# Performance work log

Measured on AMD Instinct MI355X. Metric: run time of the kernel, lower is better.

## Reference

```python
import jax, jax.numpy as jnp
from jax import lax
import numpy as np

B, T, H, W = 8, 32, 128, 128
D_MODEL, D_STATE, D_CONV, EXPAND = 256, 16, 4, 2
D_INNER = EXPAND * D_MODEL
DT_RANK = 16  # ceil(d_model/16)
CHANS = [3, 32, 64, 96]
COV_SCALE = 0.01


def setup_inputs() -> dict:
    key = jax.random.key(0)
    ks = iter(jax.random.split(key, 64))
    def n(shape, s=0.02):
        return jax.random.normal(next(ks), shape, dtype=jnp.float32) * s
    inp = {
        "frames": jax.random.normal(next(ks), (B, T, 3, H, W), dtype=jnp.float32),
        "target_bboxes": jax.random.uniform(next(ks), (B, T, 4), dtype=jnp.float32),
    }
    for i in range(3):
        inp[f"conv_w{i}"] = n((CHANS[i + 1], CHANS[i], 3, 3, 3))
        inp[f"conv_b{i}"] = jnp.zeros((CHANS[i + 1],), jnp.float32)
        inp[f"bn_g{i}"] = jnp.ones((CHANS[i + 1],), jnp.float32)
        inp[f"bn_b{i}"] = jnp.zeros((CHANS[i + 1],), jnp.float32)
    inp["ep_w"] = n((D_MODEL, CHANS[-1])); inp["ep_b"] = jnp.zeros((D_MODEL,), jnp.float32)
    inp["bp1_w"] = n((64, 4), 0.1); inp["bp1_b"] = jnp.zeros((64,), jnp.float32)
    inp["bp2_w"] = n((D_MODEL, 64)); inp["bp2_b"] = jnp.zeros((D_MODEL,), jnp.float32)
    inp["in_proj_w"] = n((2 * D_INNER, D_MODEL))
    inp["conv1d_w"] = n((D_INNER, 1, D_CONV), 0.1)
    inp["conv1d_b"] = jnp.zeros((D_INNER,), jnp.float32)
    inp["x_proj_w"] = n((DT_RANK + 2 * D_STATE, D_INNER))
    inp["dt_proj_w"] = n((D_INNER, DT_RANK), 0.1)
    inp["dt_proj_b"] = jnp.full((D_INNER,), -3.0, jnp.float32)
    inp["A_log"] = jnp.log(jnp.broadcast_to(jnp.arange(1, D_STATE + 1, dtype=jnp.float32), (D_INNER, D_STATE)))
    inp["D_param"] = jnp.ones((D_INNER,), jnp.float32)
    inp["out_proj_w"] = n((D_MODEL, D_INNER))
    inp["h1_w"] = n((D_MODEL // 2, D_MODEL)); inp["h1_b"] = jnp.zeros((D_MODEL // 2,), jnp.float32)
    inp["h2_w"] = n((4, D_MODEL // 2), 0.1); inp["h2_b"] = jnp.zeros((4,), jnp.float32)
    inp["kf_F"] = jnp.eye(4, dtype=jnp.float32) + n((4, 4), 0.01)
    inp["kf_H"] = jnp.eye(4, dtype=jnp.float32) + n((4, 4), 0.01)
    inp["kf_log_q"] = n((4,), 1.0) - 2.0
    inp["kf_log_r"] = n((4,), 1.0) - 2.0
    return inp


DN3D = ("NCDHW", "OIDHW", "NCDHW")


def _forward(frames, target_bboxes, conv_w0, conv_b0, bn_g0, bn_b0,
             conv_w1, conv_b1, bn_g1, bn_b1, conv_w2, conv_b2, bn_g2, bn_b2,
             ep_w, ep_b, bp1_w, bp1_b, bp2_w, bp2_b,
             in_proj_w, conv1d_w, conv1d_b, x_proj_w, dt_proj_w, dt_proj_b,
             A_log, D_param, out_proj_w, h1_w, h1_b, h2_w, h2_b,
             kf_F, kf_H, kf_log_q, kf_log_r):
    Bn, Tn = frames.shape[0], frames.shape[1]

    # ---- bbox_proj: Linear(4,64) -> ReLU -> Linear(64,d_model) ----
    bf = jax.nn.relu(target_bboxes @ bp1_w.T + bp1_b) @ bp2_w.T + bp2_b  # (B,T,Dm)

    # ---- 3D conv encoder (BN in eval mode: running stats 0/1 -> affine only) ----
    x = jnp.transpose(frames, (0, 2, 1, 3, 4))  # (B,C,T,H,W)
    for (w, b, g, be) in ((conv_w0, conv_b0, bn_g0, bn_b0),
                          (conv_w1, conv_b1, bn_g1, bn_b1),
                          (conv_w2, conv_b2, bn_g2, bn_b2)):
        x = lax.conv_general_dilated(x, w, (1, 2, 2), ((1, 1), (1, 1), (1, 1)),
                                     dimension_numbers=DN3D) + b[None, :, None, None, None]
        x = g[None, :, None, None, None] * x + be[None, :, None, None, None]
        x = jax.nn.relu(x)
        x = lax.reduce_window(x, -jnp.inf, lax.max, (1, 1, 1, 2, 2), (1, 1, 1, 2, 2), "VALID")
    x = x.mean(axis=(3, 4))                    # AdaptiveAvgPool3d((None,1,1)) -> (B,Cenc,T)
    ff = jnp.transpose(x, (0, 2, 1)) @ ep_w.T + ep_b  # (B,T,Dm)

    u = ff + bf

    # ---- Mamba block ----
    xz = u @ in_proj_w.T                        # (B,T,2*Di)
    xm, z = jnp.split(xz, 2, axis=-1)
    xc = jnp.transpose(xm, (0, 2, 1))           # (B,Di,T)
    xc = lax.conv_general_dilated(xc, conv1d_w, (1,), ((D_CONV - 1, 0),),
                                  dimension_numbers=("NCW", "OIW", "NCW"),
                                  feature_group_count=D_INNER) + conv1d_b[None, :, None]
    xs = jax.nn.silu(jnp.transpose(xc, (0, 2, 1)))  # (B,T,Di)
    xdbl = xs @ x_proj_w.T
    dt, Bm, Cm = jnp.split(xdbl, [DT_RANK, DT_RANK + D_STATE], axis=-1)
    dt = jax.nn.softplus(dt @ dt_proj_w.T + dt_proj_b)    # (B,T,Di)
    A = -jnp.exp(A_log)                                    # (Di,Ds)
    dA = jnp.exp(dt[..., None] * A)                        # (B,T,Di,Ds)
    dBx = dt[..., None] * Bm[:, :, None, :] * xs[..., None]

    def ssm_step(h, inputs):
        dA_t, dBx_t, C_t = inputs
        h = dA_t * h + dBx_t                               # (B,Di,Ds)
        y = jnp.einsum("bds,bs->bd", h, C_t)
        return h, y

    h0 = jnp.zeros((Bn, D_INNER, D_STATE), xs.dtype)
    _, ys = lax.scan(ssm_step, h0, (jnp.transpose(dA, (1, 0, 2, 3)),
                                    jnp.transpose(dBx, (1, 0, 2, 3)),
                                    jnp.transpose(Cm, (1, 0, 2))))
    y = jnp.transpose(ys, (1, 0, 2)) + D_param * xs
    y = y * jax.nn.silu(z)
    mo = y @ out_proj_w.T                                  # (B,T,Dm)

    # ---- measurement head ----
    meas = jax.nn.sigmoid(jax.nn.relu(mo @ h1_w.T + h1_b) @ h2_w.T + h2_b)  # (B,T,4)

    # ---- Kalman filter over T (scan) ----
    Q = jnp.diag(jnp.exp(kf_log_q) + 1e-6)
    R = jnp.diag(jnp.exp(kf_log_r) + 1e-6)
    I4 = jnp.eye(4, dtype=meas.dtype)
    Hb = jnp.broadcast_to(kf_H, (Bn, 4, 4))

    def kf_step(carry, m_t):
        s, P = carry
        s_pred = jnp.einsum("ij,bjk->bik", kf_F, s)
        P_pred = jnp.einsum("ij,bjk,lk->bil", kf_F, P, kf_F) + Q
        yres = m_t - jnp.einsum("ij,bjk->bik", kf_H, s_pred)
        S = jnp.einsum("ij,bjk,lk->bil", kf_H, P_pred, kf_H) + R
        SinvH = jnp.linalg.solve(S, Hb)                    # S^{-1} H
        K = jnp.einsum("bij,bkj->bik", P_pred, SinvH)      # P H^T S^{-T}
        s_new = s_pred + K @ yres
        IKH = I4 - K @ kf_H
        P_new = IKH @ P_pred @ jnp.swapaxes(IKH, -1, -2) + (K @ R) @ jnp.swapaxes(K, -1, -2)
        return (s_new, P_new), s_new[..., 0]

    state0 = target_bboxes[:, 0, :, None]                  # (B,4,1)
    cov0 = jnp.broadcast_to(I4 * COV_SCALE, (Bn, 4, 4))
    _, preds = lax.scan(kf_step, (state0, cov0), jnp.transpose(meas, (1, 0, 2))[..., None])
    kf_pred = jnp.transpose(preds, (1, 0, 2))              # (B,T,4)
    return kf_pred, meas


def reference(frames, target_bboxes, conv_w0, conv_b0, bn_g0, bn_b0,
              conv_w1, conv_b1, bn_g1, bn_b1, conv_w2, conv_b2, bn_g2, bn_b2,
              ep_w, ep_b, bp1_w, bp1_b, bp2_w, bp2_b,
              in_proj_w, conv1d_w, conv1d_b, x_proj_w, dt_proj_w, dt_proj_b,
              A_log, D_param, out_proj_w, h1_w, h1_b, h2_w, h2_b,
              kf_F, kf_H, kf_log_q, kf_log_r):
    return _forward(frames, target_bboxes, conv_w0, conv_b0, bn_g0, bn_b0,
                    conv_w1, conv_b1, bn_g1, bn_b1, conv_w2, conv_b2, bn_g2, bn_b2,
                    ep_w, ep_b, bp1_w, bp1_b, bp2_w, bp2_b,
                    in_proj_w, conv1d_w, conv1d_b, x_proj_w, dt_proj_w, dt_proj_b,
                    A_log, D_param, out_proj_w, h1_w, h1_b, h2_w, h2_b,
                    kf_F, kf_H, kf_log_q, kf_log_r)
```

## Files before the change

### kernel.cpp

```cpp
#include <hip/hip_runtime.h>
#include <math.h>

constexpr int Bn = 8, Tn = 32;
constexpr int D_INNER = 512;

typedef __attribute__((ext_vector_type(8))) short short8;
typedef __attribute__((ext_vector_type(8))) unsigned short ushort8;
typedef __attribute__((ext_vector_type(4))) float f32x4;

__device__ inline unsigned short f2bf(float x) {
    unsigned int u = __float_as_uint(x);
    unsigned int r = (u + 0x7FFF + ((u >> 16) & 1)) >> 16;
    return (unsigned short)r;
}

__global__ void prep_all(
    const float* __restrict__ cw0, const float* __restrict__ cw1,
    const float* __restrict__ cw2,
    const float* __restrict__ ip, const float* __restrict__ xp,
    const float* __restrict__ dt, const float* __restrict__ op,
    const float* __restrict__ h1, const float* __restrict__ h2,
    const float* __restrict__ ep, const float* __restrict__ bp2,
    const float* __restrict__ bp1,
    unsigned short* __restrict__ w0b, unsigned short* __restrict__ w1b,
    unsigned short* __restrict__ w2b, float* __restrict__ tW)
{
    int idx = blockIdx.x * blockDim.x + threadIdx.x;
    if (idx < 9216) {
        int d = idx;
        int sl = d & 7, sq = (d >> 3) & 3, co = (d >> 5) & 31;
        int r = d >> 10; int ky = r % 3, kt = r / 3;
        int q = sq ^ (co & 3) ^ ((co >> 2) & 3);
        float v = 0.f;
        if (q < 3 && sl < 3)
            v = cw0[((((size_t)co * 3 + sl) * 3 + kt) * 3 + ky) * 3 + q];
        w0b[d] = f2bf(v);
    } else if (idx < 64512) {
        int d = idx - 9216;
        int sl = d & 7, sg = (d >> 3) & 3, co = (d >> 5) & 63;
        int r = d >> 11; int k9 = r % 9, kt = r / 9;
        int ci = (sg ^ (co & 3)) * 8 + sl;
        w1b[d] = f2bf(cw1[((size_t)(co * 32 + ci) * 3 + kt) * 9 + k9]);
    } else if (idx < 230400) {
        int d = idx - 64512;
        int cip = d & 31; int rest = d >> 5;
        int co = rest % 96; rest /= 96;
        int k9 = rest % 9; int hh = rest / 9;
        int h = hh & 1, kt = hh >> 1;
        int ci = h * 32 + cip;
        w2b[d] = f2bf(cw2[((size_t)(co * 64 + ci) * 3 + kt) * 9 + k9]);
    } else if (idx < 730880) {
        int d = idx - 230400;
        const float* src; int N, K, base;
        if      (d < 262144) { src = ip;  N = 1024; K = 256; base = 0; }
        else if (d < 286720) { src = xp;  N = 48;   K = 512; base = 262144; }
        else if (d < 294912) { src = dt;  N = 512;  K = 16;  base = 286720; }
        else if (d < 425984) { src = op;  N = 256;  K = 512; base = 294912; }
        else if (d < 458752) { src = h1;  N = 128;  K = 256; base = 425984; }
        else if (d < 459264) { src = h2;  N = 4;    K = 128; base = 458752; }
        else if (d < 483840) { src = ep;  N = 256;  K = 96;  base = 459264; }
        else if (d < 500224) { src = bp2; N = 256;  K = 64;  base = 483840; }
        else                 { src = bp1; N = 64;   K = 4;   base = 500224; }
        int s = d - base;
        int o = s / K, k = s - o * K;
        tW[base + k * N + o] = src[s];
    }
}

constexpr int C0_STR  = 68;
constexpr int C0_BLKS = 17 * C0_STR;

__device__ inline void conv0_fill(unsigned short* dst, const float* __restrict__ in,
                                  int b, int ts, int yt, int xh, int tid)
{
    bool tok = (ts >= 0 && ts < Tn);
    const float* src = in + (size_t)(b * Tn + (tok ? ts : 0)) * 3 * 16384;
    for (int e = tid; e < C0_BLKS; e += 512) {
        int r = e / C0_STR, c = e - r * C0_STR;
        int gy = 16 * yt - 1 + r;
        int x  = 64 * xh + c - 1;
        bool ok = tok && gy >= 0 && gy < 128 && x >= 0 && x < 128;
        float v0 = 0.f, v1 = 0.f, v2 = 0.f;
        if (ok) {
            const float* p = src + gy * 128 + x;
            v0 = p[0]; v1 = p[16384]; v2 = p[32768];
        }
        ushort8 pk = (ushort8)0;
        pk[0] = f2bf(v0); pk[1] = f2bf(v1); pk[2] = f2bf(v2);
        *(ushort8*)(dst + (size_t)e * 8) = pk;
    }
}

__global__ __launch_bounds__(512) void conv0_kernel(
    const float* __restrict__ in, const unsigned short* __restrict__ w0b,
    const float* __restrict__ bias, const float* __restrict__ gam,
    const float* __restrict__ bet, unsigned short* __restrict__ out)
{
    int tid  = threadIdx.x;
    int lane = tid & 63;
    int wv   = __builtin_amdgcn_readfirstlane(tid >> 6);
    int q    = lane >> 4;
    int l15  = lane & 15;
    int pyp  = wv >> 1;
    int hx   = wv & 1;
    int bI = blockIdx.x;
    int bt = bI >> 4, yt = (bI >> 1) & 7, xh = bI & 1;
    int b = bt >> 5, t = bt & 31;

    __shared__ __align__(16) unsigned short S[2][C0_BLKS * 8];
    __shared__ __align__(16) unsigned short W[9 * 32 * 32];

    f32x4 acc[2][2];
    #pragma unroll
    for (int dy = 0; dy < 2; ++dy)
        #pragma unroll
        for (int nt = 0; nt < 2; ++nt) acc[dy][nt] = (f32x4)0.f;

    {
        const uint4* wsrc = (const uint4*)w0b;
        uint4* wdst = (uint4*)W;
        for (int e = tid; e < 1152; e += 512) wdst[e] = wsrc[e];
    }
    conv0_fill(S[0], in, b, t - 1, yt, xh, tid);
    __syncthreads();

    int oxl = hx * 16 + l15;

    for (int kt = 0; kt < 3; ++kt) {
        if (kt < 2) conv0_fill(S[(kt + 1) & 1], in, b, t + kt, yt, xh, tid);
        const unsigned short* Sb = S[kt & 1];
        #pragma unroll
        for (int ky = 0; ky < 3; ++ky) {
            short8 bfr[2];
            #pragma unroll
            for (int nt = 0; nt < 2; ++nt) {
                int co = nt * 16 + l15;
                int i16 = ((kt * 3 + ky) * 32 + co) * 4 +
                          (q ^ (co & 3) ^ ((co >> 2) & 3));
                bfr[nt] = *(const short8*)(W + (size_t)i16 * 8);
            }
            #pragma unroll
            for (int dy = 0; dy < 2; ++dy) {
                int r = 4 * pyp + 2 * dy + ky;
                short8 af = (short8)0;
                if (q < 3)
                    af = *(const short8*)(Sb + (size_t)(r * C0_STR + 2 * oxl + q) * 8);
                #pragma unroll
                for (int nt = 0; nt < 2; ++nt)
                    acc[dy][nt] = __builtin_amdgcn_mfma_f32_16x16x32_bf16(
                        af, bfr[nt], acc[dy][nt], 0, 0, 0);
            }
        }
        __syncthreads();
    }

    unsigned short* dst = out + (size_t)bt * 32768;
    #pragma unroll
    for (int nt = 0; nt < 2; ++nt) {
        int co = nt * 16 + l15;
        float bi = bias[co], g = gam[co], be = bet[co];
        #pragma unroll
        for (int j = 0; j < 2; ++j) {
            float m0 = fmaxf(fmaf(g, acc[0][nt][2 * j]     + bi, be), 0.f);
            float m1 = fmaxf(fmaf(g, acc[0][nt][2 * j + 1] + bi, be), 0.f);
            float m2 = fmaxf(fmaf(g, acc[1][nt][2 * j]     + bi, be), 0.f);
            float m3 = fmaxf(fmaf(g, acc[1][nt][2 * j + 1] + bi, be), 0.f);
            float p = fmaxf(fmaxf(m0, m1), fmaxf(m2, m3));
            int pox = xh * 16 + hx * 8 + q * 2 + j;
            int poy = yt * 4 + pyp;
            dst[(poy * 32 + pox) * 32 + co] = f2bf(p);
        }
    }
}

__global__ __launch_bounds__(512) void conv1_kernel(
    const unsigned short* __restrict__ in, const unsigned short* __restrict__ w1b,
    const float* __restrict__ bias, const float* __restrict__ gam,
    const float* __restrict__ bet, unsigned short* __restrict__ out)
{
    int tid  = threadIdx.x;
    int lane = tid & 63;
    int wv   = tid >> 6;
    int q    = lane >> 4;
    int l15  = lane & 15;
    int oyp  = wv >> 1;
    int nh   = wv & 1;
    int bt = blockIdx.x >> 1, half = blockIdx.x & 1;
    int b = bt >> 5, t = bt & 31;

    __shared__ __align__(16) unsigned short S[17 * 34 * 32];
    __shared__ __align__(16) unsigned short W[9 * 64 * 32];

    f32x4 acc[2][2];
    #pragma unroll
    for (int mt = 0; mt < 2; ++mt)
        #pragma unroll
        for (int nt = 0; nt < 2; ++nt) acc[mt][nt] = (f32x4)0.f;

    for (int kt = 0; kt < 3; ++kt) {
        int ts = t + kt - 1;
        if (ts < 0 || ts >= Tn) continue;
        __syncthreads();
        const unsigned short* src = in + (size_t)(b * Tn + ts) * 32768;
        for (int e = tid; e < 17 * 34 * 4; e += 512) {
            int sb = e & 3;
            int pos = e >> 2;
            int ys = pos / 34, xs = pos - ys * 34;
            int g = sb ^ ((xs >> 1) & 3);
            int y = 16 * half + ys - 1, x = xs - 1;
            ushort8 v = (ushort8)0;
            if (y >= 0 && x >= 0 && x < 32)
                v = *(const ushort8*)(src + ((y * 32 + x) * 32 + g * 8));
            *(ushort8*)(S + (size_t)e * 8) = v;
        }
        {
            const uint4* wsrc = (const uint4*)(w1b + kt * 18432);
            uint4* wdst = (uint4*)W;
            for (int e = tid; e < 2304; e += 512) wdst[e] = wsrc[e];
        }
        __syncthreads();

        for (int k9 = 0; k9 < 9; ++k9) {
            int ky = k9 / 3, kx = k9 - ky * 3;
            short8 bf[2];
            #pragma unroll
            for (int nt = 0; nt < 2; ++nt) {
                int co = nh * 32 + nt * 16 + l15;
                int blk = (k9 * 64 + co) * 4 + (q ^ (co & 3));
                bf[nt] = *(const short8*)(W + blk * 8);
            }
            short8 af[2];
            #pragma unroll
            for (int mt = 0; mt < 2; ++mt) {
                int oyl = 2 * oyp + mt;
                int ys = 2 * oyl + ky;
                int xs = 2 * l15 + kx;
                int blk = (ys * 34 + xs) * 4 + (q ^ ((xs >> 1) & 3));
                af[mt] = *(const short8*)(S + blk * 8);
            }
            #pragma unroll
            for (int mt = 0; mt < 2; ++mt)
                #pragma unroll
                for (int nt = 0; nt < 2; ++nt)
                    acc[mt][nt] = __builtin_amdgcn_mfma_f32_16x16x32_bf16(
                        af[mt], bf[nt], acc[mt][nt], 0, 0, 0);
        }
    }

    unsigned short* dst = out + (size_t)bt * 4096;
    #pragma unroll
    for (int nt = 0; nt < 2; ++nt) {
        int co = nh * 32 + nt * 16 + l15;
        float bi = bias[co], g = gam[co], be = bet[co];
        #pragma unroll
        for (int j = 0; j < 2; ++j) {
            float m0 = fmaxf(fmaf(g, acc[0][nt][2 * j]     + bi, be), 0.f);
            float m1 = fmaxf(fmaf(g, acc[0][nt][2 * j + 1] + bi, be), 0.f);
            float m2 = fmaxf(fmaf(g, acc[1][nt][2 * j]     + bi, be), 0.f);
            float m3 = fmaxf(fmaf(g, acc[1][nt][2 * j + 1] + bi, be), 0.f);
            float p = fmaxf(fmaxf(m0, m1), fmaxf(m2, m3));
            int px = 2 * q + j, py = half * 4 + oyp;
            dst[(py * 8 + px) * 64 + co] = f2bf(p);
        }
    }
}

__global__ __launch_bounds__(384) void conv2_kernel(
    const unsigned short* __restrict__ in, const unsigned short* __restrict__ w2b,
    const float* __restrict__ bias, const float* __restrict__ gam,
    const float* __restrict__ bet, float* __restrict__ out)
{
    int tid  = threadIdx.x;
    int lane = tid & 63;
    int wv   = tid >> 6;
    int q    = lane >> 4;
    int l15  = lane & 15;
    int bt = blockIdx.x;
    int b = bt >> 5, t = bt & 31;

    __shared__ __align__(16) unsigned short W[864 * 5 * 8];
    __shared__ __align__(16) unsigned short S[81 * 5 * 8];

    f32x4 acc = (f32x4)0.f;

    for (int kt = 0; kt < 3; ++kt) {
        int ts = t + kt - 1;
        if (ts < 0 || ts >= Tn) continue;
        for (int h = 0; h < 2; ++h) {
            __syncthreads();
            const unsigned short* wsrc = w2b + (size_t)((kt * 2 + h) * 9) * 96 * 32;
            for (int e = tid; e < 3456; e += 384) {
                int r = e >> 2, qq = e & 3;
                uint4 v = *(const uint4*)(wsrc + r * 32 + qq * 8);
                *(uint4*)(W + (r * 5 + qq) * 8) = v;
            }
            const unsigned short* src = in + (size_t)(b * Tn + ts) * 4096 + h * 32;
            for (int e = tid; e < 81 * 4; e += 384) {
                int cb = e & 3, p = e >> 2;
                int ys = p / 9, xs = p - ys * 9;
                int y = ys - 1, x = xs - 1;
                ushort8 v = (ushort8)0;
                if (y >= 0 && x >= 0 && y < 8 && x < 8)
                    v = *(const ushort8*)(src + ((y * 8 + x) * 64 + cb * 8));
                *(ushort8*)(S + (size_t)(p * 5 + cb) * 8) = v;
            }
            __syncthreads();

            int oy = l15 >> 2, ox = l15 & 3;
            #pragma unroll
            for (int k9 = 0; k9 < 9; ++k9) {
                int ky = k9 / 3, kx = k9 - ky * 3;
                short8 bf = *(const short8*)(W + (size_t)((k9 * 96 + wv * 16 + l15) * 5 + q) * 8);
                int p = (2 * oy + ky) * 9 + (2 * ox + kx);
                short8 af = *(const short8*)(S + (size_t)(p * 5 + q) * 8);
                acc = __builtin_amdgcn_mfma_f32_16x16x32_bf16(af, bf, acc, 0, 0, 0);
            }
        }
    }

    int co = wv * 16 + l15;
    float bi = bias[co], g = gam[co], be = bet[co];
    float v0 = fmaxf(fmaf(g, acc[0] + bi, be), 0.f);
    float v1 = fmaxf(fmaf(g, acc[1] + bi, be), 0.f);
    float v2 = fmaxf(fmaf(g, acc[2] + bi, be), 0.f);
    float v3 = fmaxf(fmaf(g, acc[3] + bi, be), 0.f);
    float p0 = fmaxf(v0, v1);
    float p1 = fmaxf(v2, v3);
    float r0 = fmaxf(p0, __shfl_xor(p0, 16));
    float r1 = fmaxf(p1, __shfl_xor(p1, 16));
    if ((q & 1) == 0) {
        int py = q >> 1;
        float* o = out + (size_t)(bt * 96 + co) * 4 + py * 2;
        o[0] = r0;
        o[1] = r1;
    }
}

__global__ __launch_bounds__(256) void fuse_u_inproj(
    const float* __restrict__ buf2, const float* __restrict__ epT,
    const float* __restrict__ ep_b, const float* __restrict__ bb,
    const float* __restrict__ bp1T, const float* __restrict__ bp1_b,
    const float* __restrict__ bp2T, const float* __restrict__ bp2_b,
    const float* __restrict__ ipwT, float* __restrict__ xzb)
{
    int bt = blockIdx.x;
    int m  = threadIdx.x;
    __shared__ float hs[64];
    __shared__ float gap[96];
    __shared__ float u_lds[256];
    if (m < 64) {
        float a = bp1_b[m];
        #pragma unroll
        for (int k = 0; k < 4; ++k) a = fmaf(bp1T[k * 64 + m], bb[bt * 4 + k], a);
        hs[m] = fmaxf(a, 0.f);
    } else if (m < 160) {
        int c = m - 64;
        const float* p = buf2 + ((size_t)bt * 96 + c) * 4;
        gap[c] = 0.25f * (p[0] + p[1] + p[2] + p[3]);
    }
    __syncthreads();
    float ff = ep_b[m];
    for (int c = 0; c < 96; ++c) ff = fmaf(gap[c], epT[c * 256 + m], ff);
    float bfv = bp2_b[m];
    for (int j = 0; j < 64; ++j) bfv = fmaf(hs[j], bp2T[j * 256 + m], bfv);
    u_lds[m] = ff + bfv;
    __syncthreads();

    const float4* wbase = (const float4*)ipwT + m;
    float4 acc = {0.f, 0.f, 0.f, 0.f};
    for (int k = 0; k < 256; ++k) {
        float uk = u_lds[k];
        float4 w4 = wbase[(size_t)k * 256];
        acc.x = fmaf(uk, w4.x, acc.x);
        acc.y = fmaf(uk, w4.y, acc.y);
        acc.z = fmaf(uk, w4.z, acc.z);
        acc.w = fmaf(uk, w4.w, acc.w);
    }
    *(float4*)(xzb + (size_t)bt * 1024 + 4 * m) = acc;
}

__global__ __launch_bounds__(512) void convxd_kernel(
    const float* __restrict__ xzb, const float* __restrict__ c1w,
    const float* __restrict__ c1b, const float* __restrict__ xpw,
    const float* __restrict__ dtwT, const float* __restrict__ dt_b,
    float* __restrict__ xsb, float* __restrict__ xdb, float* __restrict__ dtbf)
{
    int bt = blockIdx.x;
    int b = bt >> 5, t = bt & 31;
    int tid = threadIdx.x;
    __shared__ float xs_lds[512];
    __shared__ float xd_lds[48];

    {
        float acc = c1b[tid];
        #pragma unroll
        for (int k = 0; k < 4; ++k) {
            int ts = t - 3 + k;
            if (ts >= 0)
                acc = fmaf(c1w[tid * 4 + k], xzb[(size_t)(b * Tn + ts) * 1024 + tid], acc);
        }
        float v = acc / (1.f + expf(-acc));
        xs_lds[tid] = v;
        xsb[(size_t)bt * 512 + tid] = v;
    }
    __syncthreads();

    {
        int wv = tid >> 6, ln = tid & 63;
        #pragma unroll
        for (int u = 0; u < 6; ++u) {
            int o = wv * 6 + u;
            const float* wrow = xpw + (size_t)o * 512;
            float acc = 0.f;
            #pragma unroll
            for (int e = 0; e < 8; ++e)
                acc = fmaf(wrow[ln + 64 * e], xs_lds[ln + 64 * e], acc);
            acc += __shfl_xor(acc, 32); acc += __shfl_xor(acc, 16);
            acc += __shfl_xor(acc, 8);  acc += __shfl_xor(acc, 4);
            acc += __shfl_xor(acc, 2);  acc += __shfl_xor(acc, 1);
            if (ln == 0) {
                xd_lds[o] = acc;
                xdb[(size_t)bt * 48 + o] = acc;
            }
        }
    }
    __syncthreads();

    {
        float a = dt_b[tid];
        #pragma unroll
        for (int k = 0; k < 16; ++k) a = fmaf(xd_lds[k], dtwT[k * 512 + tid], a);
        a = (a > 20.f) ? a : log1pf(expf(a));
        dtbf[(size_t)bt * 512 + tid] = a;
    }
}

__global__ __launch_bounds__(256) void ssm_kernel(
    const float* __restrict__ xdbl, const float* __restrict__ dtb,
    const float* __restrict__ xs, const float* __restrict__ xz,
    const float* __restrict__ A_log, const float* __restrict__ Dp,
    float* __restrict__ y)
{
    int tid = threadIdx.x;
    int lane = tid & 63;
    int s = lane & 15, dsub = lane >> 4;
    int gid = blockIdx.x * 4 + (tid >> 6);
    int b = gid >> 7;
    int d = ((gid & 127) << 2) + dsub;

    float A = -expf(A_log[d * 16 + s]);
    float Dv = Dp[d];
    float h = 0.f;
    for (int t = 0; t < Tn; ++t) {
        int bt = b * Tn + t;
        float dtv = dtb[(size_t)bt * 512 + d];
        float xv  = xs [(size_t)bt * 512 + d];
        float Bs  = xdbl[(size_t)bt * 48 + 16 + s];
        float Cs  = xdbl[(size_t)bt * 48 + 32 + s];
        float dA = expf(dtv * A);
        h = fmaf(dA, h, dtv * Bs * xv);
        float c = h * Cs;
        c += __shfl_xor(c, 8, 16);
        c += __shfl_xor(c, 4, 16);
        c += __shfl_xor(c, 2, 16);
        c += __shfl_xor(c, 1, 16);
        if (s == 0) {
            float zv = xz[(size_t)bt * 1024 + 512 + d];
            float sig = 1.f / (1.f + expf(-zv));
            y[(size_t)bt * 512 + d] = (c + Dv * xv) * (zv * sig);
        }
    }
}

__global__ __launch_bounds__(256) void out_head_kernel(
    const float* __restrict__ yb, const float* __restrict__ opwT,
    const float* __restrict__ h1wT, const float* __restrict__ h1_b,
    const float* __restrict__ h2w, const float* __restrict__ h2_b,
    float* __restrict__ meas_out)
{
    int bt = blockIdx.x;
    int m  = threadIdx.x;
    __shared__ float y_lds[512];
    __shared__ float mo_lds[256];
    __shared__ float hid_lds[128];

    y_lds[m]       = yb[(size_t)bt * 512 + m];
    y_lds[m + 256] = yb[(size_t)bt * 512 + m + 256];
    __syncthreads();

    {
        float a = 0.f;
        for (int k = 0; k < 512; ++k) a = fmaf(y_lds[k], opwT[k * 256 + m], a);
        mo_lds[m] = a;
    }
    __syncthreads();

    if (m < 128) {
        float a = h1_b[m];
        for (int k = 0; k < 256; ++k) a = fmaf(mo_lds[k], h1wT[k * 128 + m], a);
        hid_lds[m] = fmaxf(a, 0.f);
    }
    __syncthreads();

    if (m < 64) {
        int o2 = m >> 4, l15 = m & 15;
        float acc = 0.f;
        #pragma unroll
        for (int e = 0; e < 8; ++e)
            acc = fmaf(h2w[o2 * 128 + l15 + 16 * e], hid_lds[l15 + 16 * e], acc);
        acc += __shfl_xor(acc, 8, 16);
        acc += __shfl_xor(acc, 4, 16);
        acc += __shfl_xor(acc, 2, 16);
        acc += __shfl_xor(acc, 1, 16);
        if (l15 == 0) {
            float a = acc + h2_b[o2];
            meas_out[bt * 4 + o2] = 1.f / (1.f + expf(-a));
        }
    }
}

__device__ __forceinline__ float kf_mm(float Av, float Bv, int i, int j, int gb) {
    float c = 0.f;
    #pragma unroll
    for (int k = 0; k < 4; ++k)
        c = fmaf(__shfl(Av, gb + i * 4 + k, 64), __shfl(Bv, gb + k * 4 + j, 64), c);
    return c;
}
__device__ __forceinline__ float kf_mmT(float Av, float Bv, int i, int j, int gb) {
    float c = 0.f;
    #pragma unroll
    for (int k = 0; k < 4; ++k)
        c = fmaf(__shfl(Av, gb + i * 4 + k, 64), __shfl(Bv, gb + j * 4 + k, 64), c);
    return c;
}

__global__ __launch_bounds__(128) void kf_kernel(
    const float* __restrict__ meas, const float* __restrict__ bb,
    const float* __restrict__ Fin, const float* __restrict__ Hmin,
    const float* __restrict__ lq, const float* __restrict__ lr,
    float* __restrict__ pred)
{
    int tid = threadIdx.x;
    int b   = tid >> 4;
    int l16 = tid & 15;
    int i = l16 >> 2, j = l16 & 3;
    int gb = tid & 48;

    float Fv = Fin[l16], Hv = Hmin[l16];
    float R4[4];
    #pragma unroll
    for (int k = 0; k < 4; ++k) R4[k] = expf(lr[k]) + 1e-6f;
    float qi = expf(lq[i]) + 1e-6f;

    float sv = bb[b * 128 + j];
    float Pv = (i == j) ? 0.01f : 0.f;

    for (int t = 0; t < Tn; ++t) {
        float mv = meas[(b * Tn + t) * 4 + j];
        float tr = Fv * sv;
        tr += __shfl_xor(tr, 1); tr += __shfl_xor(tr, 2);
        float spv = tr;
        float spj = __shfl(spv, gb + j * 4, 64);
        float FPv = kf_mm(Fv, Pv, i, j, gb);
        float Ppv = kf_mmT(FPv, Fv, i, j, gb) + ((i == j) ? qi : 0.f);
        float hsp = Hv * spj;
        hsp += __shfl_xor(hsp, 1); hsp += __shfl_xor(hsp, 2);
        float yrv = mv - __shfl(hsp, gb + j * 4, 64);
        float HPv = kf_mm(Hv, Ppv, i, j, gb);
        float Sv = kf_mmT(HPv, Hv, i, j, gb) + ((i == j) ? R4[i] : 0.f);
        float Xv = Hv;
        #pragma unroll
        for (int c = 0; c < 4; ++c) {
            float piv = __shfl(Sv, gb + c * 5, 64);
            float dinv = 1.f / piv;
            if (i == c) { Sv *= dinv; Xv *= dinv; }
            float Scj = __shfl(Sv, gb + c * 4 + j, 64);
            float Xcj = __shfl(Xv, gb + c * 4 + j, 64);
            float f = __shfl(Sv, gb + i * 4 + c, 64);
            if (i != c) { Sv = fmaf(-f, Scj, Sv); Xv = fmaf(-f, Xcj, Xv); }
        }
        float Kv = kf_mmT(Ppv, Xv, i, j, gb);
        float t3 = Kv * yrv;
        t3 += __shfl_xor(t3, 1); t3 += __shfl_xor(t3, 2);
        float snv = spv + t3;
        if (j == 0) pred[(b * Tn + t) * 4 + i] = snv;
        float IKHv = ((i == j) ? 1.f : 0.f) - kf_mm(Kv, Hv, i, j, gb);
        float T1v = kf_mm(IKHv, Ppv, i, j, gb);
        float krk = 0.f;
        #pragma unroll
        for (int k = 0; k < 4; ++k)
            krk = fmaf(__shfl(Kv, gb + i * 4 + k, 64) * R4[k],
                       __shfl(Kv, gb + j * 4 + k, 64), krk);
        Pv = kf_mmT(T1v, IKHv, i, j, gb) + krk;
        sv = __shfl(snv, gb + j * 4, 64);
    }
}

extern "C" void kernel_launch(void* const* d_in, const int* in_sizes, int n_in,
                              void* d_out, int out_size, void* d_ws, size_t ws_size,
                              hipStream_t stream)
{
    const float* frames = (const float*)d_in[0];
    const float* bb     = (const float*)d_in[1];
    const float* cw0 = (const float*)d_in[2],  *cb0 = (const float*)d_in[3];
    const float* g0  = (const float*)d_in[4],  *be0 = (const float*)d_in[5];
    const float* cw1 = (const float*)d_in[6],  *cb1 = (const float*)d_in[7];
    const float* g1  = (const float*)d_in[8],  *be1 = (const float*)d_in[9];
    const float* cw2 = (const float*)d_in[10], *cb2 = (const float*)d_in[11];
    const float* g2  = (const float*)d_in[12], *be2 = (const float*)d_in[13];
    const float* ep_w  = (const float*)d_in[14], *ep_b  = (const float*)d_in[15];
    const float* bp1_w = (const float*)d_in[16], *bp1_b = (const float*)d_in[17];
    const float* bp2_w = (const float*)d_in[18], *bp2_b = (const float*)d_in[19];
    const float* in_proj_w = (const float*)d_in[20];
    const float* c1w = (const float*)d_in[21], *c1b = (const float*)d_in[22];
    const float* x_proj_w = (const float*)d_in[23];
    const float* dt_w = (const float*)d_in[24], *dt_b = (const float*)d_in[25];
    const float* A_log = (const float*)d_in[26], *Dp = (const float*)d_in[27];
    const float* out_proj_w = (const float*)d_in[28];
    const float* h1_w = (const float*)d_in[29], *h1_b = (const float*)d_in[30];
    const float* h2_w = (const float*)d_in[31], *h2_b = (const float*)d_in[32];
    const float* kfF = (const float*)d_in[33], *kfH = (const float*)d_in[34];
    const float* kfq = (const float*)d_in[35], *kfr = (const float*)d_in[36];

    float* ws   = (float*)d_ws;
    float* buf2 = ws;
    float* xzb  = buf2 + 98304;
    float* xsb  = xzb  + 262144;
    float* xdb  = xsb  + 131072;
    float* dtbf = xdb  + 12288;
    float* yb   = dtbf + 131072;
    float* tW   = yb   + 131072;
    unsigned short* buf0b = (unsigned short*)(tW + 500480);
    unsigned short* buf1b = buf0b + 8388608;
    unsigned short* w2b   = buf1b + 131072;
    unsigned short* w1b   = w2b + 165888;
    unsigned short* w0b   = w1b + 55296;

    float* ipwT = tW;
    float* dtwT = tW + 286720;
    float* opwT = tW + 294912;
    float* h1wT = tW + 425984;
    float* epwT = tW + 459264;
    float* bp2T = tW + 483840;
    float* bp1T = tW + 500224;

    float* kf_out   = (float*)d_out;
    float* meas_out = kf_out + Bn * Tn * 4;

    auto nblk = [](int n) { return dim3((unsigned)((n + 255) / 256)); };

    prep_all<<<nblk(730880), 256, 0, stream>>>(cw0, cw1, cw2,
                                               in_proj_w, x_proj_w, dt_w, out_proj_w,
                                               h1_w, h2_w, ep_w, bp2_w, bp1_w,
                                               w0b, w1b, w2b, tW);

    conv0_kernel<<<dim3(4096), 512, 0, stream>>>(frames, w0b, cb0, g0, be0, buf0b);
    conv1_kernel<<<dim3(512), 512, 0, stream>>>(buf0b, w1b, cb1, g1, be1, buf1b);
    conv2_kernel<<<dim3(256), 384, 0, stream>>>(buf1b, w2b, cb2, g2, be2, buf2);

    fuse_u_inproj<<<dim3(256), 256, 0, stream>>>(buf2, epwT, ep_b, bb, bp1T, bp1_b,
                                                 bp2T, bp2_b, ipwT, xzb);
    convxd_kernel<<<dim3(256), 512, 0, stream>>>(xzb, c1w, c1b, x_proj_w,
                                                 dtwT, dt_b, xsb, xdb, dtbf);
    ssm_kernel<<<dim3(256), 256, 0, stream>>>(xdb, dtbf, xsb, xzb, A_log, Dp, yb);
    out_head_kernel<<<dim3(256), 256, 0, stream>>>(yb, opwT, h1wT, h1_b,
                                                   h2_w, h2_b, meas_out);
    kf_kernel<<<dim3(1), 128, 0, stream>>>(meas_out, bb, kfF, kfH, kfq, kfr, kf_out);
}
```

Measured before the change: 339.9 us.

## Process 8 timesteps per conv0 block with rolling frame buffer; fuse GAP into conv2

Each conv0 block now covers 8 consecutive timesteps instead of one, keeping a 4-slot ring of input frame tiles in LDS so each frame slice is loaded once and reused across the three temporal taps, and the weight tile is loaded once per 8 outputs. Grid shrinks from 4096 to 512 blocks. Separately, conv2 now computes the global average pool itself via shuffles and writes one value per channel, so fuse_u_inproj reads pooled values directly. The risk is lower parallelism (512 blocks of 512 threads) and a serialized fill/compute loop per block.

```diff
diff --git a/kernel.cpp b/kernel.cpp
--- a/kernel.cpp
+++ b/kernel.cpp
@@ -104,72 +104,82 @@
     int pyp  = wv >> 1;
     int hx   = wv & 1;
     int bI = blockIdx.x;
-    int bt = bI >> 4, yt = (bI >> 1) & 7, xh = bI & 1;
-    int b = bt >> 5, t = bt & 31;
-
-    __shared__ __align__(16) unsigned short S[2][C0_BLKS * 8];
+    int b  = bI >> 6;
+    int yt = (bI >> 3) & 7;
+    int xh = (bI >> 2) & 1;
+    int tc = bI & 3;
+    int tbase = 8 * tc;
+
+    __shared__ __align__(16) unsigned short S[4][C0_BLKS * 8];
     __shared__ __align__(16) unsigned short W[9 * 32 * 32];
-
-    f32x4 acc[2][2];
-    #pragma unroll
-    for (int dy = 0; dy < 2; ++dy)
-        #pragma unroll
-        for (int nt = 0; nt < 2; ++nt) acc[dy][nt] = (f32x4)0.f;
 
     {
         const uint4* wsrc = (const uint4*)w0b;
         uint4* wdst = (uint4*)W;
         for (int e = tid; e < 1152; e += 512) wdst[e] = wsrc[e];
     }
-    conv0_fill(S[0], in, b, t - 1, yt, xh, tid);
+    conv0_fill(S[0], in, b, tbase - 1, yt, xh, tid);
+    conv0_fill(S[1], in, b, tbase,     yt, xh, tid);
+    conv0_fill(S[2], in, b, tbase + 1, yt, xh, tid);
     __syncthreads();
 
     int oxl = hx * 16 + l15;
 
-    for (int kt = 0; kt < 3; ++kt) {
-        if (kt < 2) conv0_fill(S[(kt + 1) & 1], in, b, t + kt, yt, xh, tid);
-        const unsigned short* Sb = S[kt & 1];
-        #pragma unroll
-        for (int ky = 0; ky < 3; ++ky) {
-            short8 bfr[2];
-            #pragma unroll
-            for (int nt = 0; nt < 2; ++nt) {
-                int co = nt * 16 + l15;
-                int i16 = ((kt * 3 + ky) * 32 + co) * 4 +
-                          (q ^ (co & 3) ^ ((co >> 2) & 3));
-                bfr[nt] = *(const short8*)(W + (size_t)i16 * 8);
-            }
-            #pragma unroll
-            for (int dy = 0; dy < 2; ++dy) {
-                int r = 4 * pyp + 2 * dy + ky;
-                short8 af = (short8)0;
-                if (q < 3)
-                    af = *(const short8*)(Sb + (size_t)(r * C0_STR + 2 * oxl + q) * 8);
+    for (int i = 0; i < 8; ++i) {
+        int t = tbase + i;
+        if (i < 7) conv0_fill(S[(i + 3) & 3], in, b, t + 2, yt, xh, tid);
+
+        f32x4 acc[2][2];
+        #pragma unroll
+        for (int dy = 0; dy < 2; ++dy)
+            #pragma unroll
+            for (int nt = 0; nt < 2; ++nt) acc[dy][nt] = (f32x4)0.f;
+
+        #pragma unroll
+        for (int kt = 0; kt < 3; ++kt) {
+            const unsigned short* Sb = S[(i + kt) & 3];
+            #pragma unroll
+            for (int ky = 0; ky < 3; ++ky) {
+                short8 bfr[2];
                 #pragma unroll
-                for (int nt = 0; nt < 2; ++nt)
-                    acc[dy][nt] = __builtin_amdgcn_mfma_f32_16x16x32_bf16(
-                        af, bfr[nt], acc[dy][nt], 0, 0, 0);
+                for (int nt = 0; nt < 2; ++nt) {
+                    int co = nt * 16 + l15;
+                    int i16 = ((kt * 3 + ky) * 32 + co) * 4 +
+                              (q ^ (co & 3) ^ ((co >> 2) & 3));
+                    bfr[nt] = *(const short8*)(W + (size_t)i16 * 8);
+                }
+                #pragma unroll
+                for (int dy = 0; dy < 2; ++dy) {
+                    int r = 4 * pyp + 2 * dy + ky;
+                    short8 af = (short8)0;
+                    if (q < 3)
+                        af = *(const short8*)(Sb + (size_t)(r * C0_STR + 2 * oxl + q) * 8);
+                    #pragma unroll
+                    for (int nt = 0; nt < 2; ++nt)
+                        acc[dy][nt] = __builtin_amdgcn_mfma_f32_16x16x32_bf16(
+                            af, bfr[nt], acc[dy][nt], 0, 0, 0);
+                }
+            }
+        }
+
+        unsigned short* dst = out + (size_t)(b * Tn + t) * 32768;
+        #pragma unroll
+        for (int nt = 0; nt < 2; ++nt) {
+            int co = nt * 16 + l15;
+            float bi = bias[co], g = gam[co], be = bet[co];
+            #pragma unroll
+            for (int j = 0; j < 2; ++j) {
+                float m0 = fmaxf(fmaf(g, acc[0][nt][2 * j]     + bi, be), 0.f);
+                float m1 = fmaxf(fmaf(g, acc[0][nt][2 * j + 1] + bi, be), 0.f);
+                float m2 = fmaxf(fmaf(g, acc[1][nt][2 * j]     + bi, be), 0.f);
+                float m3 = fmaxf(fmaf(g, acc[1][nt][2 * j + 1] + bi, be), 0.f);
+                float p = fmaxf(fmaxf(m0, m1), fmaxf(m2, m3));
+                int pox = xh * 16 + hx * 8 + q * 2 + j;
+                int poy = yt * 4 + pyp;
+                dst[(poy * 32 + pox) * 32 + co] = f2bf(p);
             }
         }
         __syncthreads();
-    }
-
-    unsigned short* dst = out + (size_t)bt * 32768;
-    #pragma unroll
-    for (int nt = 0; nt < 2; ++nt) {
-        int co = nt * 16 + l15;
-        float bi = bias[co], g = gam[co], be = bet[co];
-        #pragma unroll
-        for (int j = 0; j < 2; ++j) {
-            float m0 = fmaxf(fmaf(g, acc[0][nt][2 * j]     + bi, be), 0.f);
-            float m1 = fmaxf(fmaf(g, acc[0][nt][2 * j + 1] + bi, be), 0.f);
-            float m2 = fmaxf(fmaf(g, acc[1][nt][2 * j]     + bi, be), 0.f);
-            float m3 = fmaxf(fmaf(g, acc[1][nt][2 * j + 1] + bi, be), 0.f);
-            float p = fmaxf(fmaxf(m0, m1), fmaxf(m2, m3));
-            int pox = xh * 16 + hx * 8 + q * 2 + j;
-            int poy = yt * 4 + pyp;
-            dst[(poy * 32 + pox) * 32 + co] = f2bf(p);
-        }
     }
 }
 
@@ -268,7 +278,7 @@
 __global__ __launch_bounds__(384) void conv2_kernel(
     const unsigned short* __restrict__ in, const unsigned short* __restrict__ w2b,
     const float* __restrict__ bias, const float* __restrict__ gam,
-    const float* __restrict__ bet, float* __restrict__ out)
+    const float* __restrict__ bet, float* __restrict__ gapb)
 {
     int tid  = threadIdx.x;
     int lane = tid & 63;
@@ -328,16 +338,13 @@
     float p1 = fmaxf(v2, v3);
     float r0 = fmaxf(p0, __shfl_xor(p0, 16));
     float r1 = fmaxf(p1, __shfl_xor(p1, 16));
-    if ((q & 1) == 0) {
-        int py = q >> 1;
-        float* o = out + (size_t)(bt * 96 + co) * 4 + py * 2;
-        o[0] = r0;
-        o[1] = r1;
-    }
+    float gsum = r0 + r1;
+    gsum += __shfl_xor(gsum, 32);
+    if (q == 0) gapb[(size_t)bt * 96 + co] = 0.25f * gsum;
 }
 
 __global__ __launch_bounds__(256) void fuse_u_inproj(
-    const float* __restrict__ buf2, const float* __restrict__ epT,
+    const float* __restrict__ gapb, const float* __restrict__ epT,
     const float* __restrict__ ep_b, const float* __restrict__ bb,
     const float* __restrict__ bp1T, const float* __restrict__ bp1_b,
     const float* __restrict__ bp2T, const float* __restrict__ bp2_b,
@@ -354,9 +361,7 @@
         for (int k = 0; k < 4; ++k) a = fmaf(bp1T[k * 64 + m], bb[bt * 4 + k], a);
         hs[m] = fmaxf(a, 0.f);
     } else if (m < 160) {
-        int c = m - 64;
-        const float* p = buf2 + ((size_t)bt * 96 + c) * 4;
-        gap[c] = 0.25f * (p[0] + p[1] + p[2] + p[3]);
+        gap[m - 64] = gapb[(size_t)bt * 96 + (m - 64)];
     }
     __syncthreads();
     float ff = ep_b[m];
@@ -623,8 +628,8 @@
     const float* kfq = (const float*)d_in[35], *kfr = (const float*)d_in[36];
 
     float* ws   = (float*)d_ws;
-    float* buf2 = ws;
-    float* xzb  = buf2 + 98304;
+    float* gapb = ws;
+    float* xzb  = gapb + 24576;
     float* xsb  = xzb  + 262144;
     float* xdb  = xsb  + 131072;
     float* dtbf = xdb  + 12288;
@@ -654,11 +659,11 @@
                                                h1_w, h2_w, ep_w, bp2_w, bp1_w,
                                                w0b, w1b, w2b, tW);
 
-    conv0_kernel<<<dim3(4096), 512, 0, stream>>>(frames, w0b, cb0, g0, be0, buf0b);
+    conv0_kernel<<<dim3(512), 512, 0, stream>>>(frames, w0b, cb0, g0, be0, buf0b);
     conv1_kernel<<<dim3(512), 512, 0, stream>>>(buf0b, w1b, cb1, g1, be1, buf1b);
-    conv2_kernel<<<dim3(256), 384, 0, stream>>>(buf1b, w2b, cb2, g2, be2, buf2);
-
-    fuse_u_inproj<<<dim3(256), 256, 0, stream>>>(buf2, epwT, ep_b, bb, bp1T, bp1_b,
+    conv2_kernel<<<dim3(256), 384, 0, stream>>>(buf1b, w2b, cb2, g2, be2, gapb);
+
+    fuse_u_inproj<<<dim3(256), 256, 0, stream>>>(gapb, epwT, ep_b, bb, bp1T, bp1_b,
                                                  bp2T, bp2_b, ipwT, xzb);
     convxd_kernel<<<dim3(256), 512, 0, stream>>>(xzb, c1w, c1b, x_proj_w,
                                                  dtwT, dt_b, xsb, xdb, dtbf);
```

Measured after the change: 341.3 us. Within noise of the previous version (+0.4%).
